# Kernel optimization log

Measured on AMD Instinct MI355X. Metric: run time of the kernel, lower is better.

The kernel has to match this reference:

```python
import jax, jax.numpy as jnp
import numpy as np

B, L, F, DM, H, DFF, NL, PRED = 8, 1000, 7, 512, 8, 2048, 4, 50
DK = DM // H           # head dim 64
P = DK // 4            # learned-mask proj dim 16
EPS = 1e-5
SCALE = 1.0 / float(np.sqrt(DK))


def _ln(x, g, b):
    m = jnp.mean(x, -1, keepdims=True)
    v = jnp.mean((x - m) ** 2, -1, keepdims=True)
    return (x - m) / jnp.sqrt(v + EPS) * g + b


def _make_pe():
    pos = np.arange(L, dtype=np.float32)[:, None]
    div = np.exp(np.arange(0, DM, 2, dtype=np.float32) * (-np.log(10000.0) / DM))
    pe = np.zeros((L, DM), dtype=np.float32)
    pe[:, 0::2] = np.sin(pos * div)
    pe[:, 1::2] = np.cos(pos * div)
    return jnp.asarray(pe)


def setup_inputs() -> dict:
    key = jax.random.key(0)
    ks = iter(jax.random.split(key, 40))
    def w(shape, s=0.02):
        return jax.random.normal(next(ks), shape, jnp.float32) * s
    return {
        "x": jax.random.normal(next(ks), (B, L, F), jnp.float32),
        "emb_w": w((F, DM)), "emb_b": jnp.zeros((DM,), jnp.float32),
        "pe": _make_pe(),
        "Wq": w((NL, DM, DM)), "bq": jnp.zeros((NL, DM), jnp.float32),
        "Wk": w((NL, DM, DM)), "bk": jnp.zeros((NL, DM), jnp.float32),
        "Wv": w((NL, DM, DM)), "bv": jnp.zeros((NL, DM), jnp.float32),
        "Wo": w((NL, DM, DM)), "bo": jnp.zeros((NL, DM), jnp.float32),
        "W1": w((NL, DM, DFF)), "b1": jnp.zeros((NL, DFF), jnp.float32),
        "W2": w((NL, DFF, DM)), "b2": jnp.zeros((NL, DM), jnp.float32),
        "g1": jnp.ones((NL, DM), jnp.float32), "be1": jnp.zeros((NL, DM), jnp.float32),
        "g2": jnp.ones((NL, DM), jnp.float32), "be2": jnp.zeros((NL, DM), jnp.float32),
        "lm_qw": w((DK, P)), "lm_qb": jnp.zeros((P,), jnp.float32),
        "lm_kw": w((DK, P)), "lm_kb": jnp.zeros((P,), jnp.float32),
        "gn": jnp.ones((DM,), jnp.float32), "bn": jnp.zeros((DM,), jnp.float32),
        "fc_w": w((DM, PRED)), "fc_b": jnp.zeros((PRED,), jnp.float32),
    }


def reference(x, emb_w, emb_b, pe, Wq, bq, Wk, bk, Wv, bv, Wo, bo,
              W1, b1, W2, b2, g1, be1, g2, be2,
              lm_qw, lm_qb, lm_kw, lm_kb, gn, bn, fc_w, fc_b):
    # eval mode: dropout = identity
    h = x @ emb_w + emb_b + pe[None]                 # [B,L,DM]
    for i in range(NL):
        q = (h @ Wq[i] + bq[i]).reshape(B, L, H, DK)
        k = (h @ Wk[i] + bk[i]).reshape(B, L, H, DK)
        v = (h @ Wv[i] + bv[i]).reshape(B, L, H, DK)
        scores = jnp.einsum('blhd,bshd->bhls', q, k) * SCALE
        # shared LearnedMask: per-head Q/K projection to P dims, tanh bias
        qp = q @ lm_qw + lm_qb                       # [B,L,H,P]
        kp = k @ lm_kw + lm_kb                       # [B,S,H,P]
        scores = scores + jnp.tanh(jnp.einsum('blhp,bshp->bhls', qp, kp))
        attn = jax.nn.softmax(scores, axis=-1)       # mask_flag=False: no mask
        ctx = jnp.einsum('bhls,bshd->blhd', attn, v).reshape(B, L, DM)
        h = _ln(h + ctx @ Wo[i] + bo[i], g1[i], be1[i])
        y = jax.nn.relu(h @ W1[i] + b1[i]) @ W2[i] + b2[i]
        h2 = _ln(h + y, g2[i], be2[i])
        h = _ln(h2 + y, g2[i], be2[i])               # module applies norm2 twice
    h = _ln(h, gn, bn)                               # Encoder final norm
    return h[:, -1, :] @ fc_w + fc_b                 # [B, PRED]
```

## Files before the change

kernel.cpp:

```cpp
#include <hip/hip_runtime.h>
#include <math.h>

#define B_    8
#define L_    1000
#define F_    7
#define DM_   512
#define H_    8
#define DFF_  2048
#define NL_   4
#define PRED_ 50
#define DK_   64
#define P_    16
#define EPS_  1e-5f
#define QKVS  1792

#define L2E_   1.4426950408889634f
#define C_QS   0.18033688011112042f
#define BS_QP  2.8853900817779268f
#define SHFT_  24.0f

typedef unsigned short u16;
typedef __bf16 bf16x8 __attribute__((ext_vector_type(8)));
typedef float  f32x4  __attribute__((ext_vector_type(4)));

__device__ inline float wave_reduce_sum(float x) {
#pragma unroll
  for (int off = 32; off >= 1; off >>= 1) x += __shfl_xor(x, off, 64);
  return x;
}
__device__ inline u16 f2bf(float f) {
  unsigned int u = __float_as_uint(f);
  unsigned int r = u + 0x7FFFu + ((u >> 16) & 1u);
  return (u16)(r >> 16);
}
__device__ inline unsigned int pack2(float a, float b) {
  return (unsigned int)f2bf(a) | ((unsigned int)f2bf(b) << 16);
}
__device__ inline float bf2f(u16 u) { return __uint_as_float(((unsigned int)u) << 16); }
__device__ inline float fexp2(float x) { return __builtin_amdgcn_exp2f(x); }
__device__ inline float frcp(float x) { return __builtin_amdgcn_rcpf(x); }

union bfrag { bf16x8 b; uint4 q; u16 u[8]; };

__device__ inline void gload16(const u16* g, u16* l) {
  __builtin_amdgcn_global_load_lds(
      (const __attribute__((address_space(1))) void*)g,
      (__attribute__((address_space(3))) void*)l, 16, 0, 0);
}

__global__ __launch_bounds__(256)
void transpose_w(const float* __restrict__ in, u16* __restrict__ out,
                 int K, int N, size_t in_lstride, size_t out_lstride,
                 int row_off, int out_ld) {
  __shared__ float tile[32][33];
  int z = blockIdx.z;
  int kk0 = blockIdx.y * 32, nn0 = blockIdx.x * 32;
  int tx = threadIdx.x & 31, ty = threadIdx.x >> 5;
  const float* ip = in + z * in_lstride;
  u16* op = out + z * out_lstride;
#pragma unroll
  for (int i = 0; i < 4; i++)
    tile[ty + i * 8][tx] = ip[(size_t)(kk0 + ty + i * 8) * N + nn0 + tx];
  __syncthreads();
#pragma unroll
  for (int i = 0; i < 4; i++)
    op[(size_t)(row_off + nn0 + ty + i * 8) * out_ld + kk0 + tx] = f2bf(tile[tx][ty + i * 8]);
}

__global__ __launch_bounds__(256)
void wfuse_kernel(const float* __restrict__ Wq, const float* __restrict__ Wk,
                  const float* __restrict__ lmqw, const float* __restrict__ lmkw,
                  u16* __restrict__ Wt) {
  int hh = blockIdx.x, side = blockIdx.y, layer = blockIdx.z;
  const float* W = (side ? Wk : Wq) + (size_t)layer * 512 * 512;
  const float* lw = side ? lmkw : lmqw;
  float scale = side ? 1.0f : BS_QP;
  __shared__ float lws[64][17];
  int t = threadIdx.x;
  for (int i = t; i < 1024; i += 256) lws[i >> 4][i & 15] = lw[i];
  __syncthreads();
  int p = t & 15, kk = t >> 4;
  u16* orow = Wt + (size_t)layer * QKVS * 512 + (size_t)(1536 + side * 128 + hh * 16 + p) * 512;
  for (int kb = 0; kb < 32; kb++) {
    int k = kb * 16 + kk;
    const float* wr = W + (size_t)k * 512 + hh * 64;
    float acc = 0.f;
#pragma unroll
    for (int d = 0; d < 64; d++) acc = fmaf(wr[d], lws[d][p], acc);
    orow[k] = f2bf(acc * scale);
  }
}

__global__ __launch_bounds__(256)
void concat_bias(const float* __restrict__ bq, const float* __restrict__ bk,
                 const float* __restrict__ bv,
                 const float* __restrict__ lmqw, const float* __restrict__ lmqb,
                 const float* __restrict__ lmkw, const float* __restrict__ lmkb,
                 float* __restrict__ bqkv) {
  int i = blockIdx.x * 256 + threadIdx.x;
  int l = i / QKVS, j = i % QKVS;
  float v;
  if (j < 512) v = bq[l * 512 + j];
  else if (j < 1024) v = bk[l * 512 + j - 512];
  else if (j < 1536) v = bv[l * 512 + j - 1024];
  else if (j < 1664) {
    int hh = (j - 1536) >> 4, p = (j - 1536) & 15;
    float acc = lmqb[p];
#pragma unroll
    for (int d = 0; d < 64; d++) acc = fmaf(bq[l * 512 + hh * 64 + d], lmqw[d * 16 + p], acc);
    v = acc * BS_QP;
  } else {
    int hh = (j - 1664) >> 4, p = (j - 1664) & 15;
    float acc = lmkb[p];
#pragma unroll
    for (int d = 0; d < 64; d++) acc = fmaf(bk[l * 512 + hh * 64 + d], lmkw[d * 16 + p], acc);
    v = acc;
  }
  bqkv[i] = v;
}

__global__ __launch_bounds__(512)
void embed_kernel(const float* __restrict__ x, const float* __restrict__ emb_w,
                  const float* __restrict__ emb_b, const float* __restrict__ pe,
                  u16* __restrict__ h16) {
  int bl = blockIdx.x;
  int l = bl % L_;
  int d = threadIdx.x;
  const float* xr = x + (size_t)bl * F_;
  float acc = emb_b[d] + pe[(size_t)l * DM_ + d];
#pragma unroll
  for (int f = 0; f < F_; f++) acc = fmaf(xr[f], emb_w[f * DM_ + d], acc);
  h16[(size_t)bl * DM_ + d] = f2bf(acc);
}

template<int BN>
__global__ __launch_bounds__(256)
void gemm16(const u16* __restrict__ A, const u16* __restrict__ Bt,
            const float* __restrict__ bias, const u16* __restrict__ resid,
            u16* __restrict__ C16, u16* __restrict__ vtg,
            int M, int K, int N, int relu, int nscale, float sval) {
  constexpr int NTW = BN / 32;
  constexpr int BG  = BN / 32;
  __shared__ u16 As[128 * 64];
  __shared__ u16 Bs[BN * 64];
  int t = threadIdx.x;
  int w = t >> 6, lane = t & 63;
  int wr = w >> 1, wc = w & 1;
  int mloc = lane & 15, quad = lane >> 4;
  int m0 = blockIdx.y * 128, n0 = blockIdx.x * BN;

  const u16* agp[4]; u16* alds[4];
#pragma unroll
  for (int j = 0; j < 4; j++) {
    int r = w * 32 + j * 8 + (lane >> 3);
    int gm = m0 + r; if (gm > M - 1) gm = M - 1;
    int ch = (lane & 7) ^ (r & 7);
    agp[j] = A + (size_t)gm * K + ch * 8;
    alds[j] = As + (w * 32 + j * 8) * 64;
  }
  const u16* bgp[BG]; u16* blds[BG];
#pragma unroll
  for (int j = 0; j < BG; j++) {
    int r = w * (8 * BG) + j * 8 + (lane >> 3);
    int ch = (lane & 7) ^ (r & 7);
    bgp[j] = Bt + (size_t)(n0 + r) * K + ch * 8;
    blds[j] = Bs + (w * (8 * BG) + j * 8) * 64;
  }
  const u16* apt[2][4];
#pragma unroll
  for (int mi = 0; mi < 4; mi++) {
    int tr = wr * 64 + mi * 16 + mloc;
    apt[0][mi] = As + tr * 64 + ((quad ^ (tr & 7)) * 8);
    apt[1][mi] = As + tr * 64 + (((4 + quad) ^ (tr & 7)) * 8);
  }
  const u16* bpt[2][NTW];
#pragma unroll
  for (int nt = 0; nt < NTW; nt++) {
    int tr = wc * (BN / 2) + nt * 16 + mloc;
    bpt[0][nt] = Bs + tr * 64 + ((quad ^ (tr & 7)) * 8);
    bpt[1][nt] = Bs + tr * 64 + (((4 + quad) ^ (tr & 7)) * 8);
  }

  f32x4 acc[4][NTW];
#pragma unroll
  for (int mi = 0; mi < 4; mi++)
#pragma unroll
    for (int nt = 0; nt < NTW; nt++) acc[mi][nt] = (f32x4){0.f, 0.f, 0.f, 0.f};

  for (int k0 = 0; k0 < K; k0 += 64) {
    __syncthreads();
#pragma unroll
    for (int j = 0; j < 4; j++) gload16(agp[j] + k0, alds[j]);
#pragma unroll
    for (int j = 0; j < BG; j++) gload16(bgp[j] + k0, blds[j]);
    __syncthreads();
#pragma unroll
    for (int kc = 0; kc < 2; kc++) {
      bf16x8 af[4], bv[NTW];
#pragma unroll
      for (int mi = 0; mi < 4; mi++) af[mi] = *(const bf16x8*)apt[kc][mi];
#pragma unroll
      for (int nt = 0; nt < NTW; nt++) bv[nt] = *(const bf16x8*)bpt[kc][nt];
#pragma unroll
      for (int mi = 0; mi < 4; mi++)
#pragma unroll
        for (int nt = 0; nt < NTW; nt++)
          acc[mi][nt] = __builtin_amdgcn_mfma_f32_16x16x32_bf16(af[mi], bv[nt], acc[mi][nt], 0, 0, 0);
    }
  }

#pragma unroll
  for (int mi = 0; mi < 4; mi++) {
    int m_r0 = m0 + wr * 64 + mi * 16 + quad * 4;
#pragma unroll
    for (int nt = 0; nt < NTW; nt++) {
      int nbase = n0 + wc * (BN / 2) + nt * 16;
      int n = nbase + mloc;
      if (vtg && nbase >= 1024 && nbase < 1536) {
        if (m_r0 < M) {
          int bb = (m_r0 * 67109) >> 26;
          int ll = m_r0 - bb * 1000;
          int hh2 = (n - 1024) >> 6, dk = n & 63;
          float bn_ = bias[n];
          union { uint2 d; u16 s[4]; } pk;
#pragma unroll
          for (int r = 0; r < 4; r++) pk.s[r] = f2bf(acc[mi][nt][r] + bn_);
          u16* dst = vtg + ((size_t)(bb * 8 + hh2) * 64 + dk) * 1024 + ll;
          *(uint2*)dst = pk.d;
        }
      } else {
        float bn_ = bias[n];
#pragma unroll
        for (int r = 0; r < 4; r++) {
          int m = m_r0 + r;
          if (m >= M) continue;
          size_t crow = (size_t)m * N;
          float vsum = acc[mi][nt][r] + bn_;
          if (resid) vsum += bf2f(resid[crow + n]);
          if (n < nscale) vsum *= sval;
          if (relu) vsum = fmaxf(vsum, 0.f);
          C16[crow + n] = f2bf(vsum);
        }
      }
    }
  }
}

#define KT   64
#define KPLD 24
#define PSLD 40
__global__ __launch_bounds__(256)
void attn_mfma_kernel(const u16* __restrict__ qkv, const u16* __restrict__ vtg,
                      u16* __restrict__ ctx) {
  __shared__ u16 Ks[KT * 64];
  __shared__ u16 Vt[64 * KT];
  __shared__ u16 Kp[KT * KPLD];
  __shared__ u16 Ps[4 * 16 * PSLD];

  int Lid = blockIdx.x;
  int qt = Lid >> 6;
  int bh = ((Lid & 7) << 3) | ((Lid >> 3) & 7);
  int b = bh >> 3, hh = bh & 7;
  int l0 = qt * 64;
  int t = threadIdx.x;
  int wv = t >> 6, lane = t & 63;
  int m = lane & 15, quad = lane >> 4;

  int lq = l0 + wv * 16 + m; if (lq > L_ - 1) lq = L_ - 1;
  const u16* qrow = qkv + (size_t)(b * L_ + lq) * QKVS + hh * DK_;
  bf16x8 qa0 = *(const bf16x8*)(qrow + quad * 8);
  bf16x8 qa1 = *(const bf16x8*)(qrow + 32 + quad * 8);
  bfrag qpa;
  if (quad < 2) {
    qpa.q = *(const uint4*)(qkv + (size_t)(b * L_ + lq) * QKVS + 1536 + hh * P_ + quad * 8);
  } else {
    qpa.q = make_uint4(0u, 0u, 0u, 0u);
  }

  const u16* ks_g = qkv + ((size_t)b * L_ + (t >> 3)) * QKVS + 512 + hh * DK_
                    + ((t & 7) ^ ((t >> 3) & 7)) * 8;
  u16* ks_l = Ks + (t >> 6) * 512;
  const u16* vt_g = vtg + ((size_t)bh * DK_ + (t >> 3)) * 1024
                    + ((t & 7) ^ ((t >> 3) & 7)) * 8;
  u16* vt_l = Vt + (t >> 6) * 512;

  f32x4 O[4];
#pragma unroll
  for (int nt = 0; nt < 4; nt++) O[nt] = (f32x4){0.f, 0.f, 0.f, 0.f};
  float lrun[4] = {0.f, 0.f, 0.f, 0.f};

  u16* pw = Ps + wv * (16 * PSLD);
  const u16* pr0 = pw + m * PSLD + quad * 8;
  const f32x4 zz = (f32x4){0.f, 0.f, 0.f, 0.f};

  for (int s0 = 0; s0 < L_; s0 += KT) {
    uint4 p0, p1;
    if (t < KT) {
      int sg2 = s0 + t; if (sg2 > L_ - 1) sg2 = L_ - 1;
      const u16* pr = qkv + (size_t)(b * L_ + sg2) * QKVS + 1664 + hh * P_;
      p0 = *(const uint4*)(pr);
      p1 = *(const uint4*)(pr + 8);
    }
    __syncthreads();
#pragma unroll
    for (int j = 0; j < 2; j++) {
      gload16(ks_g + ((size_t)s0 + j * 32) * QKVS, ks_l + j * 2048);
      gload16(vt_g + s0 + (size_t)j * 32 * 1024, vt_l + j * 2048);
    }
    if (t < KT) {
      *(uint4*)&Kp[t * KPLD]     = p0;
      *(uint4*)&Kp[t * KPLD + 8] = p1;
    }
    __syncthreads();

#pragma unroll
    for (int kc = 0; kc < 2; kc++) {
      float pv2[2][4];
#pragma unroll
      for (int h2 = 0; h2 < 2; h2++) {
        int nt = kc * 2 + h2;
        const u16* kb = Ks + (nt * 16 + m) * 64;
        int x0 = ((quad) ^ (m & 7)) * 8;
        int x1 = ((4 + quad) ^ (m & 7)) * 8;
        f32x4 sacc = __builtin_amdgcn_mfma_f32_16x16x32_bf16(qa0, *(const bf16x8*)(kb + x0), zz, 0, 0, 0);
        sacc = __builtin_amdgcn_mfma_f32_16x16x32_bf16(qa1, *(const bf16x8*)(kb + x1), sacc, 0, 0, 0);
        bf16x8 kpf = *(const bf16x8*)(Kp + (nt * 16 + m) * KPLD + (quad & 1) * 8);
        f32x4 macc = __builtin_amdgcn_mfma_f32_16x16x32_bf16(qpa.b, kpf, zz, 0, 0, 0);
        bool oob = (s0 + nt * 16 + m) >= L_;
#pragma unroll
        for (int r = 0; r < 4; r++) {
          float e = fexp2(macc[r]);
          float d = frcp(e + 1.f);
          float th = fmaf(d, -2.f * L2E_, L2E_);
          float s = sacc[r] + th;
          if (oob) s = -3e38f;
          float p = fexp2(s - SHFT_);
          pv2[h2][r] = p;
          lrun[r] += p;
        }
      }
#pragma unroll
      for (int h2 = 0; h2 < 2; h2++)
#pragma unroll
        for (int r = 0; r < 4; r++)
          pw[(quad * 4 + r) * PSLD + h2 * 16 + m] = f2bf(pv2[h2][r]);
      bf16x8 pa = *(const bf16x8*)pr0;
#pragma unroll
      for (int ntd = 0; ntd < 4; ntd++) {
        const u16* vb = Vt + (ntd * 16 + m) * KT + (((kc * 4 + quad) ^ (m & 7)) * 8);
        O[ntd] = __builtin_amdgcn_mfma_f32_16x16x32_bf16(pa, *(const bf16x8*)vb, O[ntd], 0, 0, 0);
      }
    }
  }

  float inv[4];
#pragma unroll
  for (int r = 0; r < 4; r++) {
#pragma unroll
    for (int msk = 1; msk < 16; msk <<= 1) lrun[r] += __shfl_xor(lrun[r], msk, 64);
    inv[r] = frcp(lrun[r]);
  }
#pragma unroll
  for (int r = 0; r < 4; r++) {
    int l = l0 + wv * 16 + quad * 4 + r;
    if (l >= L_) continue;
    u16* crow = ctx + ((size_t)(b * L_ + l)) * DM_ + hh * DK_;
#pragma unroll
    for (int nt = 0; nt < 4; nt++) crow[nt * 16 + m] = f2bf(O[nt][r] * inv[r]);
  }
}

__global__ __launch_bounds__(256)
void ln_kernel(const u16* __restrict__ a, const float* __restrict__ g,
               const float* __restrict__ be, u16* __restrict__ o) {
  int row = blockIdx.x;
  int t = threadIdx.x;
  size_t base = (size_t)row * DM_;
  unsigned int av = *(const unsigned int*)(a + base + 2 * t);
  float x0 = bf2f((u16)av), x1 = bf2f((u16)(av >> 16));
  float s = wave_reduce_sum(x0 + x1);
  float ss = wave_reduce_sum(x0 * x0 + x1 * x1);
  __shared__ float sh_s[4], sh_ss[4];
  int wv = t >> 6, lane = t & 63;
  if (lane == 0) { sh_s[wv] = s; sh_ss[wv] = ss; }
  __syncthreads();
  float S = sh_s[0] + sh_s[1] + sh_s[2] + sh_s[3];
  float SS = sh_ss[0] + sh_ss[1] + sh_ss[2] + sh_ss[3];
  float mean = S * (1.0f / DM_);
  float var = SS * (1.0f / DM_) - mean * mean;
  float rstd = rsqrtf(var + EPS_);
  float r0 = (x0 - mean) * rstd * g[2 * t] + be[2 * t];
  float r1 = (x1 - mean) * rstd * g[2 * t + 1] + be[2 * t + 1];
  *(unsigned int*)(o + base + 2 * t) = pack2(r0, r1);
}

__global__ __launch_bounds__(256)
void ln2x_kernel(const u16* __restrict__ hin, const u16* __restrict__ y,
                 const float* __restrict__ g, const float* __restrict__ be,
                 u16* __restrict__ o16) {
  int row = blockIdx.x;
  int t = threadIdx.x;
  size_t base = (size_t)row * DM_;
  unsigned int hv = *(const unsigned int*)(hin + base + 2 * t);
  unsigned int yv = *(const unsigned int*)(y + base + 2 * t);
  float y0 = bf2f((u16)yv), y1 = bf2f((u16)(yv >> 16));
  float x0 = bf2f((u16)hv) + y0, x1 = bf2f((u16)(hv >> 16)) + y1;
  __shared__ float sh_s[4], sh_ss[4];
  int wv = t >> 6, lane = t & 63;
  float g0 = g[2 * t], g1v = g[2 * t + 1], b0 = be[2 * t], b1v = be[2 * t + 1];

  float s = wave_reduce_sum(x0 + x1);
  float ss = wave_reduce_sum(x0 * x0 + x1 * x1);
  if (lane == 0) { sh_s[wv] = s; sh_ss[wv] = ss; }
  __syncthreads();
  float S = sh_s[0] + sh_s[1] + sh_s[2] + sh_s[3];
  float SS = sh_ss[0] + sh_ss[1] + sh_ss[2] + sh_ss[3];
  float mean = S * (1.0f / DM_);
  float var = SS * (1.0f / DM_) - mean * mean;
  float rstd = rsqrtf(var + EPS_);
  float h20 = (x0 - mean) * rstd * g0 + b0 + y0;
  float h21 = (x1 - mean) * rstd * g1v + b1v + y1;
  __syncthreads();

  s = wave_reduce_sum(h20 + h21);
  ss = wave_reduce_sum(h20 * h20 + h21 * h21);
  if (lane == 0) { sh_s[wv] = s; sh_ss[wv] = ss; }
  __syncthreads();
  S = sh_s[0] + sh_s[1] + sh_s[2] + sh_s[3];
  SS = sh_ss[0] + sh_ss[1] + sh_ss[2] + sh_ss[3];
  mean = S * (1.0f / DM_);
  var = SS * (1.0f / DM_) - mean * mean;
  rstd = rsqrtf(var + EPS_);
  float r0 = (h20 - mean) * rstd * g0 + b0;
  float r1 = (h21 - mean) * rstd * g1v + b1v;
  *(unsigned int*)(o16 + base + 2 * t) = pack2(r0, r1);
}

__global__ __launch_bounds__(512)
void final_kernel(const u16* __restrict__ h, const float* __restrict__ gn,
                  const float* __restrict__ bn, const float* __restrict__ fcw,
                  const float* __restrict__ fcb, float* __restrict__ out) {
  int b = blockIdx.x;
  int t = threadIdx.x;
  size_t base = ((size_t)b * L_ + (L_ - 1)) * DM_;
  float x = bf2f(h[base + t]);
  float s = wave_reduce_sum(x);
  float ss = wave_reduce_sum(x * x);
  __shared__ float sh_s[8], sh_ss[8];
  int wv = t >> 6, lane = t & 63;
  if (lane == 0) { sh_s[wv] = s; sh_ss[wv] = ss; }
  __syncthreads();
  float S = 0.f, SS = 0.f;
#pragma unroll
  for (int i = 0; i < 8; i++) { S += sh_s[i]; SS += sh_ss[i]; }
  float mean = S * (1.0f / DM_);
  float var = SS * (1.0f / DM_) - mean * mean;
  float rstd = rsqrtf(var + EPS_);
  __shared__ float hn[DM_];
  hn[t] = (x - mean) * rstd * gn[t] + bn[t];
  __syncthreads();
  if (t < PRED_) {
    float acc = fcb[t];
#pragma unroll 8
    for (int d = 0; d < DM_; d++) acc = fmaf(hn[d], fcw[d * PRED_ + t], acc);
    out[b * PRED_ + t] = acc;
  }
}

extern "C" void kernel_launch(void* const* d_in, const int* in_sizes, int n_in,
                              void* d_out, int out_size, void* d_ws, size_t ws_size,
                              hipStream_t stream) {
  const float* x     = (const float*)d_in[0];
  const float* emb_w = (const float*)d_in[1];
  const float* emb_b = (const float*)d_in[2];
  const float* pe    = (const float*)d_in[3];
  const float* Wq = (const float*)d_in[4];  const float* bq = (const float*)d_in[5];
  const float* Wk = (const float*)d_in[6];  const float* bk = (const float*)d_in[7];
  const float* Wv = (const float*)d_in[8];  const float* bv = (const float*)d_in[9];
  const float* Wo = (const float*)d_in[10]; const float* bo = (const float*)d_in[11];
  const float* W1 = (const float*)d_in[12]; const float* b1 = (const float*)d_in[13];
  const float* W2 = (const float*)d_in[14]; const float* b2 = (const float*)d_in[15];
  const float* g1 = (const float*)d_in[16]; const float* be1 = (const float*)d_in[17];
  const float* g2 = (const float*)d_in[18]; const float* be2 = (const float*)d_in[19];
  const float* lm_qw = (const float*)d_in[20]; const float* lm_qb = (const float*)d_in[21];
  const float* lm_kw = (const float*)d_in[22]; const float* lm_kb = (const float*)d_in[23];
  const float* gn = (const float*)d_in[24]; const float* bn = (const float*)d_in[25];
  const float* fc_w = (const float*)d_in[26]; const float* fc_b = (const float*)d_in[27];
  float* out = (float*)d_out;

  const size_t ROWS = (size_t)B_ * L_;
  u16* qkv16 = (u16*)d_ws;
  u16* ctx16 = qkv16 + ROWS * QKVS;
  u16* ffn1  = qkv16;
  u16* h16   = ctx16 + ROWS * DM_;
  u16* t16   = h16 + ROWS * DM_;
  u16* vtg   = t16 + ROWS * DM_;
  u16* Wqkv_t = vtg + (size_t)64 * 64 * 1024;
  u16* Wo_t   = Wqkv_t + (size_t)NL_ * QKVS * DM_;
  u16* W1_t   = Wo_t + (size_t)NL_ * DM_ * DM_;
  u16* W2_t   = W1_t + (size_t)NL_ * DFF_ * DM_;
  float* bqkv = (float*)(W2_t + (size_t)NL_ * DM_ * DFF_);

  transpose_w<<<dim3(16, 16, NL_), 256, 0, stream>>>(Wq, Wqkv_t, DM_, DM_, (size_t)DM_ * DM_, (size_t)QKVS * DM_, 0, DM_);
  transpose_w<<<dim3(16, 16, NL_), 256, 0, stream>>>(Wk, Wqkv_t, DM_, DM_, (size_t)DM_ * DM_, (size_t)QKVS * DM_, 512, DM_);
  transpose_w<<<dim3(16, 16, NL_), 256, 0, stream>>>(Wv, Wqkv_t, DM_, DM_, (size_t)DM_ * DM_, (size_t)QKVS * DM_, 1024, DM_);
  transpose_w<<<dim3(16, 16, NL_), 256, 0, stream>>>(Wo, Wo_t, DM_, DM_, (size_t)DM_ * DM_, (size_t)DM_ * DM_, 0, DM_);
  transpose_w<<<dim3(64, 16, NL_), 256, 0, stream>>>(W1, W1_t, DM_, DFF_, (size_t)DM_ * DFF_, (size_t)DFF_ * DM_, 0, DM_);
  transpose_w<<<dim3(16, 64, NL_), 256, 0, stream>>>(W2, W2_t, DFF_, DM_, (size_t)DFF_ * DM_, (size_t)DM_ * DFF_, 0, DFF_);
  wfuse_kernel<<<dim3(H_, 2, NL_), 256, 0, stream>>>(Wq, Wk, lm_qw, lm_kw, Wqkv_t);
  concat_bias<<<NL_ * QKVS / 256, 256, 0, stream>>>(bq, bk, bv, lm_qw, lm_qb, lm_kw, lm_kb, bqkv);

  embed_kernel<<<dim3((unsigned)ROWS), 512, 0, stream>>>(x, emb_w, emb_b, pe, h16);

  dim3 g_qkv(QKVS / 128, 63);
  dim3 g_ffn1(DFF_ / 128, 63);
  dim3 g_n512(DM_ / 64, 63);
  dim3 g_attn(1024);

  for (int i = 0; i < NL_; i++) {
    gemm16<128><<<g_qkv, 256, 0, stream>>>(h16, Wqkv_t + (size_t)i * QKVS * DM_,
        bqkv + i * QKVS, nullptr, qkv16, vtg, 8000, DM_, QKVS, 0, 512, C_QS);

    attn_mfma_kernel<<<g_attn, 256, 0, stream>>>(qkv16, vtg, ctx16);

    gemm16<64><<<g_n512, 256, 0, stream>>>(ctx16, Wo_t + (size_t)i * DM_ * DM_,
        bo + i * DM_, h16, t16, nullptr, 8000, DM_, DM_, 0, 0, 1.0f);
    ln_kernel<<<dim3((unsigned)ROWS), 256, 0, stream>>>(t16, g1 + i * DM_, be1 + i * DM_, h16);

    gemm16<128><<<g_ffn1, 256, 0, stream>>>(h16, W1_t + (size_t)i * DFF_ * DM_,
        b1 + i * DFF_, nullptr, ffn1, nullptr, 8000, DM_, DFF_, 1, 0, 1.0f);
    gemm16<64><<<g_n512, 256, 0, stream>>>(ffn1, W2_t + (size_t)i * DM_ * DFF_,
        b2 + i * DM_, nullptr, t16, nullptr, 8000, DFF_, DM_, 0, 0, 1.0f);

    ln2x_kernel<<<dim3((unsigned)ROWS), 256, 0, stream>>>(h16, t16, g2 + i * DM_, be2 + i * DM_, h16);
  }

  final_kernel<<<B_, 512, 0, stream>>>(h16, gn, bn, fc_w, fc_b, out);
}
```

Before: 1.091 ms.

## Prefetch GEMM and attention tiles into registers instead of direct global-to-LDS loads

Replaces the global_load_lds direct-to-LDS copies in both the GEMM and the attention kernel with register-staged software pipelining. The next K/V or A/B tile is loaded into registers while the current tile is computed, then written to LDS at the start of the next iteration. Adds s_setprio around the MFMA blocks in attention to favour matrix issue. The aim is to hide global load latency behind compute, at the cost of more VGPRs per thread and an extra register-to-LDS store step.

```diff
diff --git a/kernel.cpp b/kernel.cpp
--- a/kernel.cpp
+++ b/kernel.cpp
@@ -41,12 +41,6 @@
 __device__ inline float frcp(float x) { return __builtin_amdgcn_rcpf(x); }
 
 union bfrag { bf16x8 b; uint4 q; u16 u[8]; };
-
-__device__ inline void gload16(const u16* g, u16* l) {
-  __builtin_amdgcn_global_load_lds(
-      (const __attribute__((address_space(1))) void*)g,
-      (__attribute__((address_space(3))) void*)l, 16, 0, 0);
-}
 
 __global__ __launch_bounds__(256)
 void transpose_w(const float* __restrict__ in, u16* __restrict__ out,
@@ -140,7 +134,7 @@
             u16* __restrict__ C16, u16* __restrict__ vtg,
             int M, int K, int N, int relu, int nscale, float sval) {
   constexpr int NTW = BN / 32;
-  constexpr int BG  = BN / 32;
+  constexpr int BGN = BN / 32;
   __shared__ u16 As[128 * 64];
   __shared__ u16 Bs[BN * 64];
   int t = threadIdx.x;
@@ -158,13 +152,13 @@
     agp[j] = A + (size_t)gm * K + ch * 8;
     alds[j] = As + (w * 32 + j * 8) * 64;
   }
-  const u16* bgp[BG]; u16* blds[BG];
-#pragma unroll
-  for (int j = 0; j < BG; j++) {
-    int r = w * (8 * BG) + j * 8 + (lane >> 3);
+  const u16* bgp[BGN]; u16* blds[BGN];
+#pragma unroll
+  for (int j = 0; j < BGN; j++) {
+    int r = w * (8 * BGN) + j * 8 + (lane >> 3);
     int ch = (lane & 7) ^ (r & 7);
     bgp[j] = Bt + (size_t)(n0 + r) * K + ch * 8;
-    blds[j] = Bs + (w * (8 * BG) + j * 8) * 64;
+    blds[j] = Bs + (w * (8 * BGN) + j * 8) * 64;
   }
   const u16* apt[2][4];
 #pragma unroll
@@ -187,13 +181,27 @@
 #pragma unroll
     for (int nt = 0; nt < NTW; nt++) acc[mi][nt] = (f32x4){0.f, 0.f, 0.f, 0.f};
 
-  for (int k0 = 0; k0 < K; k0 += 64) {
+  uint4 ra[4], rb[BGN];
+#pragma unroll
+  for (int j = 0; j < 4; j++) ra[j] = *(const uint4*)(agp[j]);
+#pragma unroll
+  for (int j = 0; j < BGN; j++) rb[j] = *(const uint4*)(bgp[j]);
+
+  const int nk = K >> 6;
+  for (int tt = 0; tt < nk; ++tt) {
     __syncthreads();
 #pragma unroll
-    for (int j = 0; j < 4; j++) gload16(agp[j] + k0, alds[j]);
-#pragma unroll
-    for (int j = 0; j < BG; j++) gload16(bgp[j] + k0, blds[j]);
+    for (int j = 0; j < 4; j++) *(uint4*)(alds[j] + (lane << 3)) = ra[j];
+#pragma unroll
+    for (int j = 0; j < BGN; j++) *(uint4*)(blds[j] + (lane << 3)) = rb[j];
     __syncthreads();
+    if (tt + 1 < nk) {
+      const int koff = (tt + 1) * 64;
+#pragma unroll
+      for (int j = 0; j < 4; j++) ra[j] = *(const uint4*)(agp[j] + koff);
+#pragma unroll
+      for (int j = 0; j < BGN; j++) rb[j] = *(const uint4*)(bgp[j] + koff);
+    }
 #pragma unroll
     for (int kc = 0; kc < 2; kc++) {
       bf16x8 af[4], bv[NTW];
@@ -293,25 +301,43 @@
   const u16* pr0 = pw + m * PSLD + quad * 8;
   const f32x4 zz = (f32x4){0.f, 0.f, 0.f, 0.f};
 
-  for (int s0 = 0; s0 < L_; s0 += KT) {
-    uint4 p0, p1;
+  uint4 ka0 = {}, ka1 = {}, va0 = {}, va1 = {}, p0 = {}, p1 = {};
+  {
+    ka0 = *(const uint4*)(ks_g);
+    ka1 = *(const uint4*)(ks_g + (size_t)32 * QKVS);
+    va0 = *(const uint4*)(vt_g);
+    va1 = *(const uint4*)(vt_g + 32 * 1024);
     if (t < KT) {
-      int sg2 = s0 + t; if (sg2 > L_ - 1) sg2 = L_ - 1;
-      const u16* pr = qkv + (size_t)(b * L_ + sg2) * QKVS + 1664 + hh * P_;
+      const u16* pr = qkv + (size_t)(b * L_ + t) * QKVS + 1664 + hh * P_;
       p0 = *(const uint4*)(pr);
       p1 = *(const uint4*)(pr + 8);
     }
+  }
+
+  for (int s0 = 0; s0 < L_; s0 += KT) {
     __syncthreads();
-#pragma unroll
-    for (int j = 0; j < 2; j++) {
-      gload16(ks_g + ((size_t)s0 + j * 32) * QKVS, ks_l + j * 2048);
-      gload16(vt_g + s0 + (size_t)j * 32 * 1024, vt_l + j * 2048);
-    }
+    *(uint4*)(ks_l + (lane << 3))        = ka0;
+    *(uint4*)(ks_l + 2048 + (lane << 3)) = ka1;
+    *(uint4*)(vt_l + (lane << 3))        = va0;
+    *(uint4*)(vt_l + 2048 + (lane << 3)) = va1;
     if (t < KT) {
       *(uint4*)&Kp[t * KPLD]     = p0;
       *(uint4*)&Kp[t * KPLD + 8] = p1;
     }
     __syncthreads();
+    if (s0 + KT < L_) {
+      const int sn = s0 + KT;
+      ka0 = *(const uint4*)(ks_g + (size_t)sn * QKVS);
+      ka1 = *(const uint4*)(ks_g + (size_t)(sn + 32) * QKVS);
+      va0 = *(const uint4*)(vt_g + sn);
+      va1 = *(const uint4*)(vt_g + sn + 32 * 1024);
+      if (t < KT) {
+        int sg2 = sn + t; if (sg2 > L_ - 1) sg2 = L_ - 1;
+        const u16* pr = qkv + (size_t)(b * L_ + sg2) * QKVS + 1664 + hh * P_;
+        p0 = *(const uint4*)(pr);
+        p1 = *(const uint4*)(pr + 8);
+      }
+    }
 
 #pragma unroll
     for (int kc = 0; kc < 2; kc++) {
@@ -322,10 +348,14 @@
         const u16* kb = Ks + (nt * 16 + m) * 64;
         int x0 = ((quad) ^ (m & 7)) * 8;
         int x1 = ((4 + quad) ^ (m & 7)) * 8;
-        f32x4 sacc = __builtin_amdgcn_mfma_f32_16x16x32_bf16(qa0, *(const bf16x8*)(kb + x0), zz, 0, 0, 0);
-        sacc = __builtin_amdgcn_mfma_f32_16x16x32_bf16(qa1, *(const bf16x8*)(kb + x1), sacc, 0, 0, 0);
+        bf16x8 kf0 = *(const bf16x8*)(kb + x0);
+        bf16x8 kf1 = *(const bf16x8*)(kb + x1);
         bf16x8 kpf = *(const bf16x8*)(Kp + (nt * 16 + m) * KPLD + (quad & 1) * 8);
+        __builtin_amdgcn_s_setprio(1);
+        f32x4 sacc = __builtin_amdgcn_mfma_f32_16x16x32_bf16(qa0, kf0, zz, 0, 0, 0);
+        sacc = __builtin_amdgcn_mfma_f32_16x16x32_bf16(qa1, kf1, sacc, 0, 0, 0);
         f32x4 macc = __builtin_amdgcn_mfma_f32_16x16x32_bf16(qpa.b, kpf, zz, 0, 0, 0);
+        __builtin_amdgcn_s_setprio(0);
         bool oob = (s0 + nt * 16 + m) >= L_;
 #pragma unroll
         for (int r = 0; r < 4; r++) {
@@ -345,11 +375,13 @@
         for (int r = 0; r < 4; r++)
           pw[(quad * 4 + r) * PSLD + h2 * 16 + m] = f2bf(pv2[h2][r]);
       bf16x8 pa = *(const bf16x8*)pr0;
+      __builtin_amdgcn_s_setprio(1);
 #pragma unroll
       for (int ntd = 0; ntd < 4; ntd++) {
         const u16* vb = Vt + (ntd * 16 + m) * KT + (((kc * 4 + quad) ^ (m & 7)) * 8);
         O[ntd] = __builtin_amdgcn_mfma_f32_16x16x32_bf16(pa, *(const bf16x8*)vb, O[ntd], 0, 0, 0);
       }
+      __builtin_amdgcn_s_setprio(0);
     }
   }
 
```

Result: slower. 1.909 ms (+74.9%).

## Double-buffer attention K/V tiles and pass P through registers via shuffles

Applied to the files above, without the earlier changes.

The attention kernel now double-buffers K, V^T and the learned-mask key projections in LDS, prefetching the next 64-key tile while computing the current one. That removes one of the two barriers per tile. It also swaps the MFMA operands so scores come out transposed, which lets the P matrix be rebuilt as an A-fragment through wave shuffles instead of a round trip through shared memory. MFMA sections are raised in priority with s_setprio. The cost is twice the LDS footprint, which may lower occupancy, plus extra shuffle instructions.

```diff
diff --git a/kernel.cpp b/kernel.cpp
--- a/kernel.cpp
+++ b/kernel.cpp
@@ -247,15 +247,12 @@
 }
 
 #define KT   64
-#define KPLD 24
-#define PSLD 40
 __global__ __launch_bounds__(256)
 void attn_mfma_kernel(const u16* __restrict__ qkv, const u16* __restrict__ vtg,
                       u16* __restrict__ ctx) {
-  __shared__ u16 Ks[KT * 64];
-  __shared__ u16 Vt[64 * KT];
-  __shared__ u16 Kp[KT * KPLD];
-  __shared__ u16 Ps[4 * 16 * PSLD];
+  __shared__ u16 Ks[2 * KT * 64];
+  __shared__ u16 Vt[2 * 64 * KT];
+  __shared__ u16 Kp[2 * KT * 16];
 
   int Lid = blockIdx.x;
   int qt = Lid >> 6;
@@ -279,94 +276,114 @@
 
   const u16* ks_g = qkv + ((size_t)b * L_ + (t >> 3)) * QKVS + 512 + hh * DK_
                     + ((t & 7) ^ ((t >> 3) & 7)) * 8;
-  u16* ks_l = Ks + (t >> 6) * 512;
+  u16* ks_l = Ks + wv * 512;
   const u16* vt_g = vtg + ((size_t)bh * DK_ + (t >> 3)) * 1024
                     + ((t & 7) ^ ((t >> 3) & 7)) * 8;
-  u16* vt_l = Vt + (t >> 6) * 512;
+  u16* vt_l = Vt + wv * 512;
+  const u16* kp_g = qkv + ((size_t)b * L_ + (t >> 1)) * QKVS + 1664 + hh * P_
+                    + (t & 1) * 8;
+  u16* kp_l = Kp + wv * 512;
 
   f32x4 O[4];
 #pragma unroll
   for (int nt = 0; nt < 4; nt++) O[nt] = (f32x4){0.f, 0.f, 0.f, 0.f};
-  float lrun[4] = {0.f, 0.f, 0.f, 0.f};
-
-  u16* pw = Ps + wv * (16 * PSLD);
-  const u16* pr0 = pw + m * PSLD + quad * 8;
+  float lsum = 0.f;
   const f32x4 zz = (f32x4){0.f, 0.f, 0.f, 0.f};
 
-  for (int s0 = 0; s0 < L_; s0 += KT) {
-    uint4 p0, p1;
-    if (t < KT) {
-      int sg2 = s0 + t; if (sg2 > L_ - 1) sg2 = L_ - 1;
-      const u16* pr = qkv + (size_t)(b * L_ + sg2) * QKVS + 1664 + hh * P_;
-      p0 = *(const uint4*)(pr);
-      p1 = *(const uint4*)(pr + 8);
+#pragma unroll
+  for (int j = 0; j < 2; j++) {
+    gload16(ks_g + (size_t)(j * 32) * QKVS, ks_l + j * 2048);
+    gload16(vt_g + (size_t)j * 32 * 1024, vt_l + j * 2048);
+  }
+  if (wv < 2) gload16(kp_g, kp_l);
+  __syncthreads();
+
+  for (int tt = 0; tt < 16; ++tt) {
+    const int s0 = tt * KT;
+    const int c = tt & 1;
+    if (tt < 15) {
+      const int sn = s0 + KT, nb = c ^ 1;
+#pragma unroll
+      for (int j = 0; j < 2; j++) {
+        gload16(ks_g + ((size_t)sn + j * 32) * QKVS, ks_l + nb * 4096 + j * 2048);
+        gload16(vt_g + sn + (size_t)j * 32 * 1024, vt_l + nb * 4096 + j * 2048);
+      }
+      if (wv < 2) gload16(kp_g + (size_t)sn * QKVS, kp_l + nb * 1024);
     }
-    __syncthreads();
-#pragma unroll
-    for (int j = 0; j < 2; j++) {
-      gload16(ks_g + ((size_t)s0 + j * 32) * QKVS, ks_l + j * 2048);
-      gload16(vt_g + s0 + (size_t)j * 32 * 1024, vt_l + j * 2048);
+
+    const u16* Kc = Ks + c * 4096;
+    const u16* Vc = Vt + c * 4096;
+    const u16* Pc = Kp + c * 1024;
+
+    unsigned pklo[4], pkhi[4];
+#pragma unroll
+    for (int nt = 0; nt < 4; nt++) {
+      const u16* kb = Kc + (nt * 16 + m) * 64;
+      int x0 = (quad ^ (m & 7)) * 8;
+      int x1 = ((4 + quad) ^ (m & 7)) * 8;
+      bf16x8 kf0 = *(const bf16x8*)(kb + x0);
+      bf16x8 kf1 = *(const bf16x8*)(kb + x1);
+      bf16x8 kpf = *(const bf16x8*)(Pc + (nt * 16 + m) * 16 + (quad & 1) * 8);
+      __builtin_amdgcn_s_setprio(1);
+      f32x4 sacc = __builtin_amdgcn_mfma_f32_16x16x32_bf16(kf0, qa0, zz, 0, 0, 0);
+      sacc = __builtin_amdgcn_mfma_f32_16x16x32_bf16(kf1, qa1, sacc, 0, 0, 0);
+      f32x4 macc = __builtin_amdgcn_mfma_f32_16x16x32_bf16(kpf, qpa.b, zz, 0, 0, 0);
+      __builtin_amdgcn_s_setprio(0);
+      int keyb = s0 + nt * 16 + quad * 4;
+      float pv[4];
+#pragma unroll
+      for (int r = 0; r < 4; r++) {
+        float e = fexp2(macc[r]);
+        float d = frcp(e + 1.f);
+        float th = fmaf(d, -2.f * L2E_, L2E_);
+        float s = sacc[r] + th;
+        if (keyb + r >= L_) s = -3e38f;
+        float p = fexp2(s - SHFT_);
+        pv[r] = p;
+        lsum += p;
+      }
+      pklo[nt] = pack2(pv[0], pv[1]);
+      pkhi[nt] = pack2(pv[2], pv[3]);
     }
-    if (t < KT) {
-      *(uint4*)&Kp[t * KPLD]     = p0;
-      *(uint4*)&Kp[t * KPLD + 8] = p1;
+
+#pragma unroll
+    for (int ks = 0; ks < 2; ks++) {
+      int sl = m + ((quad & 1) << 5);
+      unsigned e0a = (unsigned)__shfl((int)pklo[2 * ks],     sl, 64);
+      unsigned e0b = (unsigned)__shfl((int)pklo[2 * ks + 1], sl, 64);
+      unsigned e1a = (unsigned)__shfl((int)pkhi[2 * ks],     sl, 64);
+      unsigned e1b = (unsigned)__shfl((int)pkhi[2 * ks + 1], sl, 64);
+      unsigned o0a = (unsigned)__shfl((int)pklo[2 * ks],     sl + 16, 64);
+      unsigned o0b = (unsigned)__shfl((int)pklo[2 * ks + 1], sl + 16, 64);
+      unsigned o1a = (unsigned)__shfl((int)pkhi[2 * ks],     sl + 16, 64);
+      unsigned o1b = (unsigned)__shfl((int)pkhi[2 * ks + 1], sl + 16, 64);
+      bool hi = quad >= 2;
+      bfrag af;
+      af.q.x = hi ? e0b : e0a;
+      af.q.y = hi ? e1b : e1a;
+      af.q.z = hi ? o0b : o0a;
+      af.q.w = hi ? o1b : o1a;
+      __builtin_amdgcn_s_setprio(1);
+#pragma unroll
+      for (int ntd = 0; ntd < 4; ntd++) {
+        const u16* vb = Vc + (ntd * 16 + m) * KT + (((ks * 4 + quad) ^ (m & 7)) * 8);
+        O[ntd] = __builtin_amdgcn_mfma_f32_16x16x32_bf16(af.b, *(const bf16x8*)vb, O[ntd], 0, 0, 0);
+      }
+      __builtin_amdgcn_s_setprio(0);
     }
-    __syncthreads();
-
-#pragma unroll
-    for (int kc = 0; kc < 2; kc++) {
-      float pv2[2][4];
-#pragma unroll
-      for (int h2 = 0; h2 < 2; h2++) {
-        int nt = kc * 2 + h2;
-        const u16* kb = Ks + (nt * 16 + m) * 64;
-        int x0 = ((quad) ^ (m & 7)) * 8;
-        int x1 = ((4 + quad) ^ (m & 7)) * 8;
-        f32x4 sacc = __builtin_amdgcn_mfma_f32_16x16x32_bf16(qa0, *(const bf16x8*)(kb + x0), zz, 0, 0, 0);
-        sacc = __builtin_amdgcn_mfma_f32_16x16x32_bf16(qa1, *(const bf16x8*)(kb + x1), sacc, 0, 0, 0);
-        bf16x8 kpf = *(const bf16x8*)(Kp + (nt * 16 + m) * KPLD + (quad & 1) * 8);
-        f32x4 macc = __builtin_amdgcn_mfma_f32_16x16x32_bf16(qpa.b, kpf, zz, 0, 0, 0);
-        bool oob = (s0 + nt * 16 + m) >= L_;
-#pragma unroll
-        for (int r = 0; r < 4; r++) {
-          float e = fexp2(macc[r]);
-          float d = frcp(e + 1.f);
-          float th = fmaf(d, -2.f * L2E_, L2E_);
-          float s = sacc[r] + th;
-          if (oob) s = -3e38f;
-          float p = fexp2(s - SHFT_);
-          pv2[h2][r] = p;
-          lrun[r] += p;
-        }
-      }
-#pragma unroll
-      for (int h2 = 0; h2 < 2; h2++)
-#pragma unroll
-        for (int r = 0; r < 4; r++)
-          pw[(quad * 4 + r) * PSLD + h2 * 16 + m] = f2bf(pv2[h2][r]);
-      bf16x8 pa = *(const bf16x8*)pr0;
-#pragma unroll
-      for (int ntd = 0; ntd < 4; ntd++) {
-        const u16* vb = Vt + (ntd * 16 + m) * KT + (((kc * 4 + quad) ^ (m & 7)) * 8);
-        O[ntd] = __builtin_amdgcn_mfma_f32_16x16x32_bf16(pa, *(const bf16x8*)vb, O[ntd], 0, 0, 0);
-      }
-    }
-  }
-
-  float inv[4];
-#pragma unroll
-  for (int r = 0; r < 4; r++) {
-#pragma unroll
-    for (int msk = 1; msk < 16; msk <<= 1) lrun[r] += __shfl_xor(lrun[r], msk, 64);
-    inv[r] = frcp(lrun[r]);
-  }
+    if (tt < 15) __syncthreads();
+  }
+
+  lsum += __shfl_xor(lsum, 16, 64);
+  lsum += __shfl_xor(lsum, 32, 64);
 #pragma unroll
   for (int r = 0; r < 4; r++) {
     int l = l0 + wv * 16 + quad * 4 + r;
     if (l >= L_) continue;
+    float inv = frcp(__shfl(lsum, quad * 4 + r, 64));
     u16* crow = ctx + ((size_t)(b * L_ + l)) * DM_ + hh * DK_;
 #pragma unroll
-    for (int nt = 0; nt < 4; nt++) crow[nt * 16 + m] = f2bf(O[nt][r] * inv[r]);
+    for (int nt = 0; nt < 4; nt++) crow[nt * 16 + m] = f2bf(O[nt][r] * inv);
   }
 }
 
```

After: 1.131 ms. 3.7% more time.
